# Kernel optimization log

Measured on AMD Instinct MI355X. Metric: run time of the kernel, lower is better.

## Reference

```python
import jax, jax.numpy as jnp
import numpy as np

B, N, D = 2, 2048, 1024
H, DH = 16, 64
INNER = H * DH  # 1024
EPS = 1e-5


def setup_inputs() -> dict:
    key = jax.random.key(0)
    ks = jax.random.split(key, 7)
    x = jax.random.normal(ks[0], (B, N, D), dtype=jnp.float32)
    mask = jax.random.uniform(ks[1], (B, N)) < 0.9
    mask = mask.at[:, 0].set(True)  # guarantee at least one valid key per row
    attn_bias = jax.random.normal(ks[2], (H, N, N), dtype=jnp.float32) * 0.02
    ln_w = jnp.ones((D,), dtype=jnp.float32)
    ln_b = jnp.zeros((D,), dtype=jnp.float32)
    wq = jax.random.normal(ks[3], (D, INNER), dtype=jnp.float32) * 0.02
    wkv = jax.random.normal(ks[4], (D, 2 * DH), dtype=jnp.float32) * 0.02
    wo = jax.random.normal(ks[5], (INNER, D), dtype=jnp.float32) * 0.02
    return {"x": x, "attn_bias": attn_bias, "ln_w": ln_w, "ln_b": ln_b,
            "wq": wq, "wkv": wkv, "wo": wo, "mask": mask}


def reference(x, attn_bias, ln_w, ln_b, wq, wkv, wo, mask):
    scale = DH ** -0.5
    # NOTE: in the torch module, kv_input = x BEFORE self.norm (context=None),
    # so K/V come from raw x while Q comes from LayerNorm(x).
    mu = jnp.mean(x, axis=-1, keepdims=True)
    var = jnp.var(x, axis=-1, keepdims=True)
    xn = (x - mu) / jnp.sqrt(var + EPS) * ln_w + ln_b
    q = (xn @ wq).reshape(B, N, H, DH).transpose(0, 2, 1, 3) * scale  # b h n d
    kv = x @ wkv                     # b n 2*dh (shared single KV head, MQA)
    k, v = kv[..., :DH], kv[..., DH:]
    sim = jnp.einsum('bhid,bjd->bhij', q, k) + attn_bias  # bias broadcasts over b
    mask_value = -jnp.finfo(sim.dtype).max
    sim = jnp.where(mask[:, None, None, :], sim, mask_value)
    attn = jax.nn.softmax(sim, axis=-1)
    out = jnp.einsum('bhij,bjd->bhid', attn, v)
    out = out.transpose(0, 2, 1, 3).reshape(B, N, INNER)
    return out @ wo
```

## Files before the change

### kernel.cpp

```cpp
#include <hip/hip_runtime.h>
#include <hip/hip_bf16.h>

typedef __bf16 bf16_t;
typedef __bf16 bf16x4 __attribute__((ext_vector_type(4)));
typedef __bf16 bf16x8 __attribute__((ext_vector_type(8)));
typedef float f32x4 __attribute__((ext_vector_type(4)));

static constexpr int BB    = 2;
static constexpr int SEQ   = 2048;
static constexpr int DM    = 1024;
static constexpr int NHEAD = 16;
static constexpr int HD    = 64;
static constexpr float L2E = 1.4426950408889634f;

__device__ __forceinline__ bf16x8 ld8(const bf16_t* p) {
  return *reinterpret_cast<const bf16x8*>(p);
}

__device__ __forceinline__ void gl_lds16(const bf16_t* g, bf16_t* l) {
  __builtin_amdgcn_global_load_lds(
      (const __attribute__((address_space(1))) void*)g,
      (__attribute__((address_space(3))) void*)l, 16, 0, 0);
}

__device__ __forceinline__ uint2 shfl2(uint2 v, int src) {
  uint2 r;
  r.x = (unsigned)__shfl((int)v.x, src, 64);
  r.y = (unsigned)__shfl((int)v.y, src, 64);
  return r;
}

template <typename T> __device__ __forceinline__ T cvt_out(float v);
template <> __device__ __forceinline__ float  cvt_out<float >(float v) { return v; }
template <> __device__ __forceinline__ bf16_t cvt_out<bf16_t>(float v) { return (bf16_t)v; }

__global__ __launch_bounds__(256) void transpose_cast(const float* __restrict__ in,
                                                      bf16_t* __restrict__ out,
                                                      int R, int C) {
  __shared__ float tile[32][33];
  const int c0 = blockIdx.x * 32, r0 = blockIdx.y * 32;
  const int tx = threadIdx.x & 31, ty = threadIdx.x >> 5;
#pragma unroll
  for (int y = ty; y < 32; y += 8)
    tile[y][tx] = in[(size_t)(r0 + y) * C + (c0 + tx)];
  __syncthreads();
#pragma unroll
  for (int y = ty; y < 32; y += 8)
    out[(size_t)(c0 + y) * R + (r0 + tx)] = (bf16_t)tile[tx][y];
}

__global__ __launch_bounds__(256) void row_prep(const float* __restrict__ x,
    const float* __restrict__ ln_w, const float* __restrict__ ln_b,
    const int* __restrict__ mask,
    bf16_t* __restrict__ xbf, bf16_t* __restrict__ xn, float* __restrict__ maskA) {
  const int row = blockIdx.x, t = threadIdx.x;
  __shared__ float red[8];
  const float4 xv = *reinterpret_cast<const float4*>(&x[(size_t)row * DM + t * 4]);
  float s  = xv.x + xv.y + xv.z + xv.w;
  float s2 = xv.x * xv.x + xv.y * xv.y + xv.z * xv.z + xv.w * xv.w;
#pragma unroll
  for (int off = 32; off >= 1; off >>= 1) {
    s  += __shfl_xor(s,  off, 64);
    s2 += __shfl_xor(s2, off, 64);
  }
  if ((t & 63) == 0) { red[t >> 6] = s; red[4 + (t >> 6)] = s2; }
  __syncthreads();
  s  = red[0] + red[1] + red[2] + red[3];
  s2 = red[4] + red[5] + red[6] + red[7];
  const float mu   = s * (1.0f / DM);
  const float var  = s2 * (1.0f / DM) - mu * mu;
  const float rstd = rsqrtf(var + 1e-5f);
  const float4 wv = *reinterpret_cast<const float4*>(&ln_w[t * 4]);
  const float4 bv = *reinterpret_cast<const float4*>(&ln_b[t * 4]);
  union { bf16_t h[4]; uint2 u; } p0, p1;
  p0.h[0] = (bf16_t)xv.x; p0.h[1] = (bf16_t)xv.y;
  p0.h[2] = (bf16_t)xv.z; p0.h[3] = (bf16_t)xv.w;
  p1.h[0] = (bf16_t)((xv.x - mu) * rstd * wv.x + bv.x);
  p1.h[1] = (bf16_t)((xv.y - mu) * rstd * wv.y + bv.y);
  p1.h[2] = (bf16_t)((xv.z - mu) * rstd * wv.z + bv.z);
  p1.h[3] = (bf16_t)((xv.w - mu) * rstd * wv.w + bv.w);
  *reinterpret_cast<uint2*>(&xbf[(size_t)row * DM + t * 4]) = p0.u;
  *reinterpret_cast<uint2*>(&xn [(size_t)row * DM + t * 4]) = p1.u;
  if (t == 0) maskA[row] = mask[row] ? 0.0f : -1e30f;
}

template <typename OutT>
__global__ __launch_bounds__(256) void gemm128(const bf16_t* __restrict__ A,
    const bf16_t* __restrict__ Bt, OutT* __restrict__ C,
    int M, int Nn, int K, float scale) {
  __shared__ alignas(16) bf16_t As[128 * 32];
  __shared__ alignas(16) bf16_t Bs[128 * 32];
  const int m0 = blockIdx.x * 128, n0 = blockIdx.y * 128;
  const int t = threadIdx.x, lane = t & 63, w = t >> 6;
  const int wm = (w & 1) * 64, wn = (w >> 1) * 64;
  const int l15 = lane & 15, q4 = lane >> 4;
  f32x4 acc[4][4] = {};
  const int sr = lane >> 2, sc = (lane & 3) * 8;
  const bf16_t* Ap0 = A  + (size_t)(m0 + w * 32 + sr) * K + sc;
  const bf16_t* Ap1 = Ap0 + (size_t)16 * K;
  const bf16_t* Bp0 = Bt + (size_t)(n0 + w * 32 + sr) * K + sc;
  const bf16_t* Bp1 = Bp0 + (size_t)16 * K;
  bf16_t* AsL0 = &As[(w * 32) * 32];
  bf16_t* AsL1 = &As[(w * 32 + 16) * 32];
  bf16_t* BsL0 = &Bs[(w * 32) * 32];
  bf16_t* BsL1 = &Bs[(w * 32 + 16) * 32];
  for (int k0 = 0; k0 < K; k0 += 32) {
    gl_lds16(Ap0 + k0, AsL0);
    gl_lds16(Ap1 + k0, AsL1);
    gl_lds16(Bp0 + k0, BsL0);
    gl_lds16(Bp1 + k0, BsL1);
    __syncthreads();
    bf16x8 af[4], bfr[4];
#pragma unroll
    for (int mt = 0; mt < 4; ++mt) af[mt]  = ld8(&As[(wm + mt * 16 + l15) * 32 + q4 * 8]);
#pragma unroll
    for (int nt = 0; nt < 4; ++nt) bfr[nt] = ld8(&Bs[(wn + nt * 16 + l15) * 32 + q4 * 8]);
#pragma unroll
    for (int mt = 0; mt < 4; ++mt)
#pragma unroll
      for (int nt = 0; nt < 4; ++nt)
        acc[mt][nt] = __builtin_amdgcn_mfma_f32_16x16x32_bf16(af[mt], bfr[nt], acc[mt][nt], 0, 0, 0);
    __syncthreads();
  }
#pragma unroll
  for (int mt = 0; mt < 4; ++mt)
#pragma unroll
    for (int nt = 0; nt < 4; ++nt)
#pragma unroll
      for (int r = 0; r < 4; ++r) {
        const int gm = m0 + wm + mt * 16 + q4 * 4 + r;
        const int gn = n0 + wn + nt * 16 + l15;
        C[(size_t)gm * Nn + gn] = cvt_out<OutT>(acc[mt][nt][r] * scale);
      }
}

__global__ __launch_bounds__(256) void gemm_kv(const bf16_t* __restrict__ A,
    const bf16_t* __restrict__ Bt, bf16_t* __restrict__ C, bf16_t* __restrict__ C2,
    int M, int Nn, int K) {
  __shared__ alignas(16) bf16_t As[128 * 32];
  __shared__ alignas(16) bf16_t Bs[64 * 32];
  const int m0 = blockIdx.x * 128, n0 = blockIdx.y * 64;
  const int t = threadIdx.x, lane = t & 63, w = t >> 6;
  const int wm = (w & 1) * 64, wn = (w >> 1) * 32;
  const int l15 = lane & 15, q4 = lane >> 4;
  f32x4 acc[4][2] = {};
  const int sr = lane >> 2, sc = (lane & 3) * 8;
  const bf16_t* Ap0 = A  + (size_t)(m0 + w * 32 + sr) * K + sc;
  const bf16_t* Ap1 = Ap0 + (size_t)16 * K;
  const bf16_t* Bp  = Bt + (size_t)(n0 + w * 16 + sr) * K + sc;
  bf16_t* AsL0 = &As[(w * 32) * 32];
  bf16_t* AsL1 = &As[(w * 32 + 16) * 32];
  bf16_t* BsL  = &Bs[(w * 16) * 32];
  for (int k0 = 0; k0 < K; k0 += 32) {
    gl_lds16(Ap0 + k0, AsL0);
    gl_lds16(Ap1 + k0, AsL1);
    gl_lds16(Bp  + k0, BsL);
    __syncthreads();
    bf16x8 af[4], bfr[2];
#pragma unroll
    for (int mt = 0; mt < 4; ++mt) af[mt]  = ld8(&As[(wm + mt * 16 + l15) * 32 + q4 * 8]);
#pragma unroll
    for (int nt = 0; nt < 2; ++nt) bfr[nt] = ld8(&Bs[(wn + nt * 16 + l15) * 32 + q4 * 8]);
#pragma unroll
    for (int mt = 0; mt < 4; ++mt)
#pragma unroll
      for (int nt = 0; nt < 2; ++nt)
        acc[mt][nt] = __builtin_amdgcn_mfma_f32_16x16x32_bf16(af[mt], bfr[nt], acc[mt][nt], 0, 0, 0);
    __syncthreads();
  }
#pragma unroll
  for (int mt = 0; mt < 4; ++mt)
#pragma unroll
    for (int nt = 0; nt < 2; ++nt)
#pragma unroll
      for (int r = 0; r < 4; ++r) {
        const int gm = m0 + wm + mt * 16 + q4 * 4 + r;
        const int gn = n0 + wn + nt * 16 + l15;
        const bf16_t ov = (bf16_t)acc[mt][nt][r];
        if (gn < HD) C[(size_t)gm * HD + gn] = ov;
        else C2[((size_t)(gm >> 11) * HD + (gn - HD)) * SEQ + (gm & 2047)] = ov;
      }
}

__global__ __launch_bounds__(256, 4) void flash_attn(
    const bf16_t* __restrict__ q,
    const bf16_t* __restrict__ kk,
    const bf16_t* __restrict__ vT,
    const float*  __restrict__ bias,
    const float*  __restrict__ maskA,
    bf16_t* __restrict__ aout)
{
  const int b = blockIdx.y & 1, h = blockIdx.y >> 1;
  const int i0 = blockIdx.x * 64;
  const int t = threadIdx.x, lane = t & 63, w = t >> 6;
  const int l15 = lane & 15, q4 = lane >> 4;

  __shared__ alignas(16) bf16_t Ks[2][64][72];
  __shared__ alignas(16) bf16_t Vs[2][64][72];

  const bf16_t* qrow = &q[((size_t)b * SEQ + i0 + w * 16 + l15) * DM + h * HD];
  const bf16x8 bq0 = ld8(qrow + q4 * 8);
  const bf16x8 bq1 = ld8(qrow + 32 + q4 * 8);

  f32x4 o[4] = {};
  float m_run = -1e30f, l_run = 0.0f;

  const float* bias_p = bias + (size_t)h * SEQ * SEQ
                      + (size_t)(i0 + w * 16 + l15) * SEQ + q4 * 4;
  const float* mask_p = maskA + b * SEQ + q4 * 4;

  const int sr = t >> 2, sc = (t & 3) * 16;
  const bf16_t* kp = &kk[((size_t)b * SEQ + sr) * HD + sc];
  const bf16_t* vp = &vT[((size_t)b * HD + sr) * SEQ + sc];

  uint4 kr0 = *reinterpret_cast<const uint4*>(kp);
  uint4 kr1 = *reinterpret_cast<const uint4*>(kp + 8);
  uint4 vr0 = *reinterpret_cast<const uint4*>(vp);
  uint4 vr1 = *reinterpret_cast<const uint4*>(vp + 8);
  f32x4 bv[4], mv[4];
#pragma unroll
  for (int mt = 0; mt < 4; ++mt) {
    bv[mt] = *reinterpret_cast<const f32x4*>(bias_p + mt * 16);
    mv[mt] = *reinterpret_cast<const f32x4*>(mask_p + mt * 16);
  }
  *reinterpret_cast<uint4*>(&Ks[0][sr][sc])     = kr0;
  *reinterpret_cast<uint4*>(&Ks[0][sr][sc + 8]) = kr1;
  *reinterpret_cast<uint4*>(&Vs[0][sr][sc])     = vr0;
  *reinterpret_cast<uint4*>(&Vs[0][sr][sc + 8]) = vr1;
  __syncthreads();

  for (int it = 0; it < SEQ / 64; ++it) {
    const int buf = it & 1;
    const int j1 = (it + 1) * 64;
    const bool more = (j1 < SEQ);
    if (more) {
      kr0 = *reinterpret_cast<const uint4*>(kp + (size_t)j1 * HD);
      kr1 = *reinterpret_cast<const uint4*>(kp + (size_t)j1 * HD + 8);
      vr0 = *reinterpret_cast<const uint4*>(vp + j1);
      vr1 = *reinterpret_cast<const uint4*>(vp + j1 + 8);
    }

    f32x4 s[4];
#pragma unroll
    for (int mt = 0; mt < 4; ++mt) {
      const bf16x8 a0 = ld8(&Ks[buf][mt * 16 + l15][q4 * 8]);
      const bf16x8 a1 = ld8(&Ks[buf][mt * 16 + l15][32 + q4 * 8]);
      f32x4 z = {0.f, 0.f, 0.f, 0.f};
      z = __builtin_amdgcn_mfma_f32_16x16x32_bf16(a0, bq0, z, 0, 0, 0);
      z = __builtin_amdgcn_mfma_f32_16x16x32_bf16(a1, bq1, z, 0, 0, 0);
      s[mt] = z;
    }

    float mx = -1e30f;
#pragma unroll
    for (int mt = 0; mt < 4; ++mt)
#pragma unroll
      for (int r = 0; r < 4; ++r) {
        s[mt][r] = s[mt][r] + bv[mt][r] + mv[mt][r];
        mx = fmaxf(mx, s[mt][r]);
      }
    if (more) {
#pragma unroll
      for (int mt = 0; mt < 4; ++mt) {
        bv[mt] = *reinterpret_cast<const f32x4*>(bias_p + j1 + mt * 16);
        mv[mt] = *reinterpret_cast<const f32x4*>(mask_p + j1 + mt * 16);
      }
    }
    mx = fmaxf(mx, __shfl_xor(mx, 16, 64));
    mx = fmaxf(mx, __shfl_xor(mx, 32, 64));
    const float mnew  = fmaxf(m_run, mx);
    const float alpha = __builtin_amdgcn_exp2f((m_run - mnew) * L2E);
    const float cc    = -mnew * L2E;
    m_run = mnew;

    float su = 0.0f;
#pragma unroll
    for (int mt = 0; mt < 4; ++mt)
#pragma unroll
      for (int r = 0; r < 4; ++r) {
        s[mt][r] = __builtin_amdgcn_exp2f(__builtin_fmaf(s[mt][r], L2E, cc));
        su += s[mt][r];
      }
    su += __shfl_xor(su, 16, 64);
    su += __shfl_xor(su, 32, 64);
    l_run = l_run * alpha + su;

#pragma unroll
    for (int r = 0; r < 4; ++r) {
      const float a_r = __shfl(alpha, q4 * 4 + r, 64);
      o[0][r] *= a_r; o[1][r] *= a_r; o[2][r] *= a_r; o[3][r] *= a_r;
    }

    uint2 pk[4];
#pragma unroll
    for (int mt = 0; mt < 4; ++mt) {
      union { bf16_t hh[4]; uint2 u; } pu;
      pu.hh[0] = (bf16_t)s[mt][0]; pu.hh[1] = (bf16_t)s[mt][1];
      pu.hh[2] = (bf16_t)s[mt][2]; pu.hh[3] = (bf16_t)s[mt][3];
      pk[mt] = pu.u;
    }
    const int src0 = ((q4 & 1) << 5) + l15;
    const int src1 = src0 + 16;
    const bool hiSel = (q4 >> 1) != 0;
#pragma unroll
    for (int ks = 0; ks < 2; ++ks) {
      const uint2 a0 = shfl2(pk[2 * ks],     src0);
      const uint2 a1 = shfl2(pk[2 * ks + 1], src0);
      const uint2 b0 = shfl2(pk[2 * ks],     src1);
      const uint2 b1 = shfl2(pk[2 * ks + 1], src1);
      union { unsigned u[4]; bf16x8 v; } pf;
      pf.u[0] = hiSel ? a1.x : a0.x; pf.u[1] = hiSel ? a1.y : a0.y;
      pf.u[2] = hiSel ? b1.x : b0.x; pf.u[3] = hiSel ? b1.y : b0.y;
#pragma unroll
      for (int nt = 0; nt < 4; ++nt) {
        const bf16x8 vv = ld8(&Vs[buf][nt * 16 + l15][ks * 32 + q4 * 8]);
        o[nt] = __builtin_amdgcn_mfma_f32_16x16x32_bf16(pf.v, vv, o[nt], 0, 0, 0);
      }
    }

    if (more) {
      *reinterpret_cast<uint4*>(&Ks[buf ^ 1][sr][sc])     = kr0;
      *reinterpret_cast<uint4*>(&Ks[buf ^ 1][sr][sc + 8]) = kr1;
      *reinterpret_cast<uint4*>(&Vs[buf ^ 1][sr][sc])     = vr0;
      *reinterpret_cast<uint4*>(&Vs[buf ^ 1][sr][sc + 8]) = vr1;
    }
    __syncthreads();
  }

#pragma unroll
  for (int r = 0; r < 4; ++r) {
    const float linv = 1.0f / __shfl(l_run, q4 * 4 + r, 64);
    const int gi = i0 + w * 16 + q4 * 4 + r;
    bf16_t* dst = &aout[((size_t)b * SEQ + gi) * DM + h * HD];
#pragma unroll
    for (int nt = 0; nt < 4; ++nt)
      dst[nt * 16 + l15] = (bf16_t)(o[nt][r] * linv);
  }
}

extern "C" void kernel_launch(void* const* d_in, const int* in_sizes, int n_in,
                              void* d_out, int out_size, void* d_ws, size_t ws_size,
                              hipStream_t stream) {
  const float* x         = (const float*)d_in[0];
  const float* attn_bias = (const float*)d_in[1];
  const float* ln_w      = (const float*)d_in[2];
  const float* ln_b      = (const float*)d_in[3];
  const float* wq        = (const float*)d_in[4];
  const float* wkv       = (const float*)d_in[5];
  const float* wo        = (const float*)d_in[6];
  const int*   mask      = (const int*)d_in[7];
  float* out = (float*)d_out;

  char* ws = (char*)d_ws;
  size_t off = 0;
  auto alloc = [&](size_t bytes) {
    char* p = ws + off;
    off += (bytes + 255) & ~(size_t)255;
    return p;
  };
  bf16_t* xbf   = (bf16_t*)alloc((size_t)BB * SEQ * DM * 2);
  bf16_t* xn    = (bf16_t*)alloc((size_t)BB * SEQ * DM * 2);
  bf16_t* wqT   = (bf16_t*)alloc((size_t)DM * DM * 2);
  bf16_t* wkvT  = (bf16_t*)alloc((size_t)2 * HD * DM * 2);
  bf16_t* woT   = (bf16_t*)alloc((size_t)DM * DM * 2);
  bf16_t* qb    = (bf16_t*)alloc((size_t)BB * SEQ * DM * 2);
  bf16_t* kkb   = (bf16_t*)alloc((size_t)BB * SEQ * HD * 2);
  bf16_t* vTb   = (bf16_t*)alloc((size_t)BB * HD * SEQ * 2);
  bf16_t* aoutb = (bf16_t*)alloc((size_t)BB * SEQ * DM * 2);
  float*  maskA = (float*)alloc((size_t)BB * SEQ * 4);

  transpose_cast<<<dim3(DM / 32, DM / 32), 256, 0, stream>>>(wq, wqT, DM, DM);
  transpose_cast<<<dim3(128 / 32, DM / 32), 256, 0, stream>>>(wkv, wkvT, DM, 128);
  transpose_cast<<<dim3(DM / 32, DM / 32), 256, 0, stream>>>(wo, woT, DM, DM);
  row_prep<<<BB * SEQ, 256, 0, stream>>>(x, ln_w, ln_b, mask, xbf, xn, maskA);
  gemm128<bf16_t><<<dim3(32, 8), 256, 0, stream>>>(xn, wqT, qb, BB * SEQ, DM, DM, 0.125f);
  gemm_kv<<<dim3(32, 2), 256, 0, stream>>>(xbf, wkvT, kkb, vTb, BB * SEQ, 128, DM);
  flash_attn<<<dim3(SEQ / 64, BB * NHEAD), 256, 0, stream>>>(qb, kkb, vTb, attn_bias,
                                                             maskA, aoutb);
  gemm128<float><<<dim3(32, 8), 256, 0, stream>>>(aoutb, woT, out, BB * SEQ, DM, DM, 1.0f);
}
```

Before: 512.2 us.

## Process both batches per attention block to share bias loads

Each flash-attention block now handles both batch elements for one head and query tile, so every attn_bias tile is loaded once and used twice. This halves the grid, doubles the per-block K/V staging and register state, and drops the K/V prefetch double buffering in favour of a single buffer per batch guarded by two barriers per iteration. The P-matrix relayout moves from cross-lane shuffles to a per-warp LDS scratch tile, and launch bounds fall from 4 to 3 blocks per SM to allow more registers. The gain on bias traffic comes at the cost of less latency hiding and lower occupancy.

```diff
diff --git a/kernel.cpp b/kernel.cpp
--- a/kernel.cpp
+++ b/kernel.cpp
@@ -21,13 +21,6 @@
   __builtin_amdgcn_global_load_lds(
       (const __attribute__((address_space(1))) void*)g,
       (__attribute__((address_space(3))) void*)l, 16, 0, 0);
-}
-
-__device__ __forceinline__ uint2 shfl2(uint2 v, int src) {
-  uint2 r;
-  r.x = (unsigned)__shfl((int)v.x, src, 64);
-  r.y = (unsigned)__shfl((int)v.y, src, 64);
-  return r;
 }
 
 template <typename T> __device__ __forceinline__ T cvt_out(float v);
@@ -182,7 +175,7 @@
       }
 }
 
-__global__ __launch_bounds__(256, 4) void flash_attn(
+__global__ __launch_bounds__(256, 3) void flash_attn(
     const bf16_t* __restrict__ q,
     const bf16_t* __restrict__ kk,
     const bf16_t* __restrict__ vT,
@@ -190,152 +183,171 @@
     const float*  __restrict__ maskA,
     bf16_t* __restrict__ aout)
 {
-  const int b = blockIdx.y & 1, h = blockIdx.y >> 1;
+  const int h  = blockIdx.y;
   const int i0 = blockIdx.x * 64;
   const int t = threadIdx.x, lane = t & 63, w = t >> 6;
   const int l15 = lane & 15, q4 = lane >> 4;
 
   __shared__ alignas(16) bf16_t Ks[2][64][72];
   __shared__ alignas(16) bf16_t Vs[2][64][72];
-
-  const bf16_t* qrow = &q[((size_t)b * SEQ + i0 + w * 16 + l15) * DM + h * HD];
-  const bf16x8 bq0 = ld8(qrow + q4 * 8);
-  const bf16x8 bq1 = ld8(qrow + 32 + q4 * 8);
-
-  f32x4 o[4] = {};
-  float m_run = -1e30f, l_run = 0.0f;
+  __shared__ alignas(16) bf16_t Pt[4][16][72];
+
+  bf16x8 bq[2][2];
+#pragma unroll
+  for (int b = 0; b < 2; ++b) {
+    const bf16_t* qrow = &q[((size_t)b * SEQ + i0 + w * 16 + l15) * DM + h * HD];
+    bq[b][0] = ld8(qrow + q4 * 8);
+    bq[b][1] = ld8(qrow + 32 + q4 * 8);
+  }
+
+  f32x4 o[2][4] = {};
+  float m_run[2] = {-1e30f, -1e30f};
+  float l_run[2] = {0.0f, 0.0f};
 
   const float* bias_p = bias + (size_t)h * SEQ * SEQ
                       + (size_t)(i0 + w * 16 + l15) * SEQ + q4 * 4;
-  const float* mask_p = maskA + b * SEQ + q4 * 4;
 
   const int sr = t >> 2, sc = (t & 3) * 16;
-  const bf16_t* kp = &kk[((size_t)b * SEQ + sr) * HD + sc];
-  const bf16_t* vp = &vT[((size_t)b * HD + sr) * SEQ + sc];
-
-  uint4 kr0 = *reinterpret_cast<const uint4*>(kp);
-  uint4 kr1 = *reinterpret_cast<const uint4*>(kp + 8);
-  uint4 vr0 = *reinterpret_cast<const uint4*>(vp);
-  uint4 vr1 = *reinterpret_cast<const uint4*>(vp + 8);
-  f32x4 bv[4], mv[4];
-#pragma unroll
-  for (int mt = 0; mt < 4; ++mt) {
-    bv[mt] = *reinterpret_cast<const f32x4*>(bias_p + mt * 16);
-    mv[mt] = *reinterpret_cast<const f32x4*>(mask_p + mt * 16);
-  }
-  *reinterpret_cast<uint4*>(&Ks[0][sr][sc])     = kr0;
-  *reinterpret_cast<uint4*>(&Ks[0][sr][sc + 8]) = kr1;
-  *reinterpret_cast<uint4*>(&Vs[0][sr][sc])     = vr0;
-  *reinterpret_cast<uint4*>(&Vs[0][sr][sc + 8]) = vr1;
+  const bf16_t* kp[2];
+  const bf16_t* vp[2];
+#pragma unroll
+  for (int b = 0; b < 2; ++b) {
+    kp[b] = &kk[((size_t)b * SEQ + sr) * HD + sc];
+    vp[b] = &vT[((size_t)b * HD + sr) * SEQ + sc];
+  }
+
+  uint4 kr[2][2], vr[2][2];
+#pragma unroll
+  for (int b = 0; b < 2; ++b) {
+    kr[b][0] = *reinterpret_cast<const uint4*>(kp[b]);
+    kr[b][1] = *reinterpret_cast<const uint4*>(kp[b] + 8);
+    vr[b][0] = *reinterpret_cast<const uint4*>(vp[b]);
+    vr[b][1] = *reinterpret_cast<const uint4*>(vp[b] + 8);
+  }
+#pragma unroll
+  for (int b = 0; b < 2; ++b) {
+    *reinterpret_cast<uint4*>(&Ks[b][sr][sc])     = kr[b][0];
+    *reinterpret_cast<uint4*>(&Ks[b][sr][sc + 8]) = kr[b][1];
+    *reinterpret_cast<uint4*>(&Vs[b][sr][sc])     = vr[b][0];
+    *reinterpret_cast<uint4*>(&Vs[b][sr][sc + 8]) = vr[b][1];
+  }
   __syncthreads();
 
   for (int it = 0; it < SEQ / 64; ++it) {
-    const int buf = it & 1;
-    const int j1 = (it + 1) * 64;
+    const int j0 = it * 64;
+    const int j1 = j0 + 64;
     const bool more = (j1 < SEQ);
     if (more) {
-      kr0 = *reinterpret_cast<const uint4*>(kp + (size_t)j1 * HD);
-      kr1 = *reinterpret_cast<const uint4*>(kp + (size_t)j1 * HD + 8);
-      vr0 = *reinterpret_cast<const uint4*>(vp + j1);
-      vr1 = *reinterpret_cast<const uint4*>(vp + j1 + 8);
+#pragma unroll
+      for (int b = 0; b < 2; ++b) {
+        kr[b][0] = *reinterpret_cast<const uint4*>(kp[b] + (size_t)j1 * HD);
+        kr[b][1] = *reinterpret_cast<const uint4*>(kp[b] + (size_t)j1 * HD + 8);
+        vr[b][0] = *reinterpret_cast<const uint4*>(vp[b] + j1);
+        vr[b][1] = *reinterpret_cast<const uint4*>(vp[b] + j1 + 8);
+      }
     }
 
-    f32x4 s[4];
-#pragma unroll
-    for (int mt = 0; mt < 4; ++mt) {
-      const bf16x8 a0 = ld8(&Ks[buf][mt * 16 + l15][q4 * 8]);
-      const bf16x8 a1 = ld8(&Ks[buf][mt * 16 + l15][32 + q4 * 8]);
-      f32x4 z = {0.f, 0.f, 0.f, 0.f};
-      z = __builtin_amdgcn_mfma_f32_16x16x32_bf16(a0, bq0, z, 0, 0, 0);
-      z = __builtin_amdgcn_mfma_f32_16x16x32_bf16(a1, bq1, z, 0, 0, 0);
-      s[mt] = z;
+    f32x4 bv[4];
+#pragma unroll
+    for (int mt = 0; mt < 4; ++mt)
+      bv[mt] = *reinterpret_cast<const f32x4*>(bias_p + j0 + mt * 16);
+
+    f32x4 s[2][4];
+#pragma unroll
+    for (int b = 0; b < 2; ++b)
+#pragma unroll
+      for (int mt = 0; mt < 4; ++mt) {
+        const bf16x8 a0 = ld8(&Ks[b][mt * 16 + l15][q4 * 8]);
+        const bf16x8 a1 = ld8(&Ks[b][mt * 16 + l15][32 + q4 * 8]);
+        f32x4 z = {0.f, 0.f, 0.f, 0.f};
+        z = __builtin_amdgcn_mfma_f32_16x16x32_bf16(a0, bq[b][0], z, 0, 0, 0);
+        z = __builtin_amdgcn_mfma_f32_16x16x32_bf16(a1, bq[b][1], z, 0, 0, 0);
+        s[b][mt] = z;
+      }
+
+#pragma unroll
+    for (int b = 0; b < 2; ++b) {
+      f32x4 mv[4];
+#pragma unroll
+      for (int mt = 0; mt < 4; ++mt)
+        mv[mt] = *reinterpret_cast<const f32x4*>(maskA + b * SEQ + j0 + mt * 16 + q4 * 4);
+
+      float mx = -1e30f;
+#pragma unroll
+      for (int mt = 0; mt < 4; ++mt)
+#pragma unroll
+        for (int r = 0; r < 4; ++r) {
+          s[b][mt][r] = s[b][mt][r] + bv[mt][r] + mv[mt][r];
+          mx = fmaxf(mx, s[b][mt][r]);
+        }
+      mx = fmaxf(mx, __shfl_xor(mx, 16, 64));
+      mx = fmaxf(mx, __shfl_xor(mx, 32, 64));
+      const float mnew  = fmaxf(m_run[b], mx);
+      const float alpha = __builtin_amdgcn_exp2f((m_run[b] - mnew) * L2E);
+      const float cc    = -mnew * L2E;
+      m_run[b] = mnew;
+
+      float su = 0.0f;
+#pragma unroll
+      for (int mt = 0; mt < 4; ++mt)
+#pragma unroll
+        for (int r = 0; r < 4; ++r) {
+          s[b][mt][r] = __builtin_amdgcn_exp2f(__builtin_fmaf(s[b][mt][r], L2E, cc));
+          su += s[b][mt][r];
+        }
+      su += __shfl_xor(su, 16, 64);
+      su += __shfl_xor(su, 32, 64);
+      l_run[b] = l_run[b] * alpha + su;
+
+#pragma unroll
+      for (int mt = 0; mt < 4; ++mt) {
+        union { bf16_t hh[4]; uint2 u; } pu;
+        pu.hh[0] = (bf16_t)s[b][mt][0]; pu.hh[1] = (bf16_t)s[b][mt][1];
+        pu.hh[2] = (bf16_t)s[b][mt][2]; pu.hh[3] = (bf16_t)s[b][mt][3];
+        *reinterpret_cast<uint2*>(&Pt[w][l15][mt * 16 + q4 * 4]) = pu.u;
+      }
+
+#pragma unroll
+      for (int r = 0; r < 4; ++r) {
+        const float a_r = __shfl(alpha, q4 * 4 + r, 64);
+        o[b][0][r] *= a_r; o[b][1][r] *= a_r; o[b][2][r] *= a_r; o[b][3][r] *= a_r;
+      }
+
+#pragma unroll
+      for (int ks = 0; ks < 2; ++ks) {
+        const bf16x8 pf = ld8(&Pt[w][l15][ks * 32 + q4 * 8]);
+#pragma unroll
+        for (int nt = 0; nt < 4; ++nt) {
+          const bf16x8 vv = ld8(&Vs[b][nt * 16 + l15][ks * 32 + q4 * 8]);
+          o[b][nt] = __builtin_amdgcn_mfma_f32_16x16x32_bf16(pf, vv, o[b][nt], 0, 0, 0);
+        }
+      }
     }
 
-    float mx = -1e30f;
-#pragma unroll
-    for (int mt = 0; mt < 4; ++mt)
-#pragma unroll
-      for (int r = 0; r < 4; ++r) {
-        s[mt][r] = s[mt][r] + bv[mt][r] + mv[mt][r];
-        mx = fmaxf(mx, s[mt][r]);
-      }
+    __syncthreads();
     if (more) {
 #pragma unroll
-      for (int mt = 0; mt < 4; ++mt) {
-        bv[mt] = *reinterpret_cast<const f32x4*>(bias_p + j1 + mt * 16);
-        mv[mt] = *reinterpret_cast<const f32x4*>(mask_p + j1 + mt * 16);
+      for (int b = 0; b < 2; ++b) {
+        *reinterpret_cast<uint4*>(&Ks[b][sr][sc])     = kr[b][0];
+        *reinterpret_cast<uint4*>(&Ks[b][sr][sc + 8]) = kr[b][1];
+        *reinterpret_cast<uint4*>(&Vs[b][sr][sc])     = vr[b][0];
+        *reinterpret_cast<uint4*>(&Vs[b][sr][sc + 8]) = vr[b][1];
       }
     }
-    mx = fmaxf(mx, __shfl_xor(mx, 16, 64));
-    mx = fmaxf(mx, __shfl_xor(mx, 32, 64));
-    const float mnew  = fmaxf(m_run, mx);
-    const float alpha = __builtin_amdgcn_exp2f((m_run - mnew) * L2E);
-    const float cc    = -mnew * L2E;
-    m_run = mnew;
-
-    float su = 0.0f;
-#pragma unroll
-    for (int mt = 0; mt < 4; ++mt)
-#pragma unroll
-      for (int r = 0; r < 4; ++r) {
-        s[mt][r] = __builtin_amdgcn_exp2f(__builtin_fmaf(s[mt][r], L2E, cc));
-        su += s[mt][r];
-      }
-    su += __shfl_xor(su, 16, 64);
-    su += __shfl_xor(su, 32, 64);
-    l_run = l_run * alpha + su;
-
+    __syncthreads();
+  }
+
+#pragma unroll
+  for (int b = 0; b < 2; ++b)
 #pragma unroll
     for (int r = 0; r < 4; ++r) {
-      const float a_r = __shfl(alpha, q4 * 4 + r, 64);
-      o[0][r] *= a_r; o[1][r] *= a_r; o[2][r] *= a_r; o[3][r] *= a_r;
+      const float linv = 1.0f / __shfl(l_run[b], q4 * 4 + r, 64);
+      const int gi = i0 + w * 16 + q4 * 4 + r;
+      bf16_t* dst = &aout[((size_t)b * SEQ + gi) * DM + h * HD];
+#pragma unroll
+      for (int nt = 0; nt < 4; ++nt)
+        dst[nt * 16 + l15] = (bf16_t)(o[b][nt][r] * linv);
     }
-
-    uint2 pk[4];
-#pragma unroll
-    for (int mt = 0; mt < 4; ++mt) {
-      union { bf16_t hh[4]; uint2 u; } pu;
-      pu.hh[0] = (bf16_t)s[mt][0]; pu.hh[1] = (bf16_t)s[mt][1];
-      pu.hh[2] = (bf16_t)s[mt][2]; pu.hh[3] = (bf16_t)s[mt][3];
-      pk[mt] = pu.u;
-    }
-    const int src0 = ((q4 & 1) << 5) + l15;
-    const int src1 = src0 + 16;
-    const bool hiSel = (q4 >> 1) != 0;
-#pragma unroll
-    for (int ks = 0; ks < 2; ++ks) {
-      const uint2 a0 = shfl2(pk[2 * ks],     src0);
-      const uint2 a1 = shfl2(pk[2 * ks + 1], src0);
-      const uint2 b0 = shfl2(pk[2 * ks],     src1);
-      const uint2 b1 = shfl2(pk[2 * ks + 1], src1);
-      union { unsigned u[4]; bf16x8 v; } pf;
-      pf.u[0] = hiSel ? a1.x : a0.x; pf.u[1] = hiSel ? a1.y : a0.y;
-      pf.u[2] = hiSel ? b1.x : b0.x; pf.u[3] = hiSel ? b1.y : b0.y;
-#pragma unroll
-      for (int nt = 0; nt < 4; ++nt) {
-        const bf16x8 vv = ld8(&Vs[buf][nt * 16 + l15][ks * 32 + q4 * 8]);
-        o[nt] = __builtin_amdgcn_mfma_f32_16x16x32_bf16(pf.v, vv, o[nt], 0, 0, 0);
-      }
-    }
-
-    if (more) {
-      *reinterpret_cast<uint4*>(&Ks[buf ^ 1][sr][sc])     = kr0;
-      *reinterpret_cast<uint4*>(&Ks[buf ^ 1][sr][sc + 8]) = kr1;
-      *reinterpret_cast<uint4*>(&Vs[buf ^ 1][sr][sc])     = vr0;
-      *reinterpret_cast<uint4*>(&Vs[buf ^ 1][sr][sc + 8]) = vr1;
-    }
-    __syncthreads();
-  }
-
-#pragma unroll
-  for (int r = 0; r < 4; ++r) {
-    const float linv = 1.0f / __shfl(l_run, q4 * 4 + r, 64);
-    const int gi = i0 + w * 16 + q4 * 4 + r;
-    bf16_t* dst = &aout[((size_t)b * SEQ + gi) * DM + h * HD];
-#pragma unroll
-    for (int nt = 0; nt < 4; ++nt)
-      dst[nt * 16 + l15] = (bf16_t)(o[nt][r] * linv);
-  }
 }
 
 extern "C" void kernel_launch(void* const* d_in, const int* in_sizes, int n_in,
@@ -375,7 +387,7 @@
   row_prep<<<BB * SEQ, 256, 0, stream>>>(x, ln_w, ln_b, mask, xbf, xn, maskA);
   gemm128<bf16_t><<<dim3(32, 8), 256, 0, stream>>>(xn, wqT, qb, BB * SEQ, DM, DM, 0.125f);
   gemm_kv<<<dim3(32, 2), 256, 0, stream>>>(xbf, wkvT, kkb, vTb, BB * SEQ, 128, DM);
-  flash_attn<<<dim3(SEQ / 64, BB * NHEAD), 256, 0, stream>>>(qb, kkb, vTb, attn_bias,
-                                                             maskA, aoutb);
+  flash_attn<<<dim3(SEQ / 64, NHEAD), 256, 0, stream>>>(qb, kkb, vTb, attn_bias,
+                                                        maskA, aoutb);
   gemm128<float><<<dim3(32, 8), 256, 0, stream>>>(aoutb, woT, out, BB * SEQ, DM, DM, 1.0f);
 }
```

After: 671.8 us. 1.31x slower.

## Merge both batches into one 512-thread attention block sharing bias tiles

Applied to the files above, without the earlier changes.

The flash attention kernel now launches one 512-thread block per (query tile, head) that covers both batches. Each group of four waves handles one batch and owns one K/V LDS buffer, so the two batches' loads of the same attn_bias rows can hit in cache together. This targets the fp32 bias stream, which dominates traffic because it is read once per batch. In exchange the K/V double buffering and bias/mask register prefetch are dropped, an extra barrier is added per iteration, and the grid has half as many blocks.

```diff
diff --git a/kernel.cpp b/kernel.cpp
--- a/kernel.cpp
+++ b/kernel.cpp
@@ -182,7 +182,7 @@
       }
 }
 
-__global__ __launch_bounds__(256, 4) void flash_attn(
+__global__ __launch_bounds__(512, 4) void flash_attn(
     const bf16_t* __restrict__ q,
     const bf16_t* __restrict__ kk,
     const bf16_t* __restrict__ vT,
@@ -190,15 +190,17 @@
     const float*  __restrict__ maskA,
     bf16_t* __restrict__ aout)
 {
-  const int b = blockIdx.y & 1, h = blockIdx.y >> 1;
+  const int h  = blockIdx.y;
   const int i0 = blockIdx.x * 64;
   const int t = threadIdx.x, lane = t & 63, w = t >> 6;
+  const int bg = w >> 2;
+  const int wl = w & 3;
   const int l15 = lane & 15, q4 = lane >> 4;
 
   __shared__ alignas(16) bf16_t Ks[2][64][72];
   __shared__ alignas(16) bf16_t Vs[2][64][72];
 
-  const bf16_t* qrow = &q[((size_t)b * SEQ + i0 + w * 16 + l15) * DM + h * HD];
+  const bf16_t* qrow = &q[((size_t)bg * SEQ + i0 + wl * 16 + l15) * DM + h * HD];
   const bf16x8 bq0 = ld8(qrow + q4 * 8);
   const bf16x8 bq1 = ld8(qrow + 32 + q4 * 8);
 
@@ -206,32 +208,27 @@
   float m_run = -1e30f, l_run = 0.0f;
 
   const float* bias_p = bias + (size_t)h * SEQ * SEQ
-                      + (size_t)(i0 + w * 16 + l15) * SEQ + q4 * 4;
-  const float* mask_p = maskA + b * SEQ + q4 * 4;
-
-  const int sr = t >> 2, sc = (t & 3) * 16;
-  const bf16_t* kp = &kk[((size_t)b * SEQ + sr) * HD + sc];
-  const bf16_t* vp = &vT[((size_t)b * HD + sr) * SEQ + sc];
+                      + (size_t)(i0 + wl * 16 + l15) * SEQ + q4 * 4;
+  const float* mask_p = maskA + bg * SEQ + q4 * 4;
+
+  const int tl = t & 255;
+  const int sr = tl >> 2, sc = (tl & 3) * 16;
+  const bf16_t* kp = &kk[((size_t)bg * SEQ + sr) * HD + sc];
+  const bf16_t* vp = &vT[((size_t)bg * HD + sr) * SEQ + sc];
 
   uint4 kr0 = *reinterpret_cast<const uint4*>(kp);
   uint4 kr1 = *reinterpret_cast<const uint4*>(kp + 8);
   uint4 vr0 = *reinterpret_cast<const uint4*>(vp);
   uint4 vr1 = *reinterpret_cast<const uint4*>(vp + 8);
-  f32x4 bv[4], mv[4];
-#pragma unroll
-  for (int mt = 0; mt < 4; ++mt) {
-    bv[mt] = *reinterpret_cast<const f32x4*>(bias_p + mt * 16);
-    mv[mt] = *reinterpret_cast<const f32x4*>(mask_p + mt * 16);
-  }
-  *reinterpret_cast<uint4*>(&Ks[0][sr][sc])     = kr0;
-  *reinterpret_cast<uint4*>(&Ks[0][sr][sc + 8]) = kr1;
-  *reinterpret_cast<uint4*>(&Vs[0][sr][sc])     = vr0;
-  *reinterpret_cast<uint4*>(&Vs[0][sr][sc + 8]) = vr1;
+  *reinterpret_cast<uint4*>(&Ks[bg][sr][sc])     = kr0;
+  *reinterpret_cast<uint4*>(&Ks[bg][sr][sc + 8]) = kr1;
+  *reinterpret_cast<uint4*>(&Vs[bg][sr][sc])     = vr0;
+  *reinterpret_cast<uint4*>(&Vs[bg][sr][sc + 8]) = vr1;
   __syncthreads();
 
   for (int it = 0; it < SEQ / 64; ++it) {
-    const int buf = it & 1;
-    const int j1 = (it + 1) * 64;
+    const int j0 = it * 64;
+    const int j1 = j0 + 64;
     const bool more = (j1 < SEQ);
     if (more) {
       kr0 = *reinterpret_cast<const uint4*>(kp + (size_t)j1 * HD);
@@ -240,11 +237,16 @@
       vr1 = *reinterpret_cast<const uint4*>(vp + j1 + 8);
     }
 
+    f32x4 bv[4];
+#pragma unroll
+    for (int mt = 0; mt < 4; ++mt)
+      bv[mt] = *reinterpret_cast<const f32x4*>(bias_p + j0 + mt * 16);
+
     f32x4 s[4];
 #pragma unroll
     for (int mt = 0; mt < 4; ++mt) {
-      const bf16x8 a0 = ld8(&Ks[buf][mt * 16 + l15][q4 * 8]);
-      const bf16x8 a1 = ld8(&Ks[buf][mt * 16 + l15][32 + q4 * 8]);
+      const bf16x8 a0 = ld8(&Ks[bg][mt * 16 + l15][q4 * 8]);
+      const bf16x8 a1 = ld8(&Ks[bg][mt * 16 + l15][32 + q4 * 8]);
       f32x4 z = {0.f, 0.f, 0.f, 0.f};
       z = __builtin_amdgcn_mfma_f32_16x16x32_bf16(a0, bq0, z, 0, 0, 0);
       z = __builtin_amdgcn_mfma_f32_16x16x32_bf16(a1, bq1, z, 0, 0, 0);
@@ -253,17 +255,12 @@
 
     float mx = -1e30f;
 #pragma unroll
-    for (int mt = 0; mt < 4; ++mt)
+    for (int mt = 0; mt < 4; ++mt) {
+      const f32x4 mv = *reinterpret_cast<const f32x4*>(mask_p + j0 + mt * 16);
 #pragma unroll
       for (int r = 0; r < 4; ++r) {
-        s[mt][r] = s[mt][r] + bv[mt][r] + mv[mt][r];
+        s[mt][r] = s[mt][r] + bv[mt][r] + mv[r];
         mx = fmaxf(mx, s[mt][r]);
-      }
-    if (more) {
-#pragma unroll
-      for (int mt = 0; mt < 4; ++mt) {
-        bv[mt] = *reinterpret_cast<const f32x4*>(bias_p + j1 + mt * 16);
-        mv[mt] = *reinterpret_cast<const f32x4*>(mask_p + j1 + mt * 16);
       }
     }
     mx = fmaxf(mx, __shfl_xor(mx, 16, 64));
@@ -313,16 +310,17 @@
       pf.u[2] = hiSel ? b1.x : b0.x; pf.u[3] = hiSel ? b1.y : b0.y;
 #pragma unroll
       for (int nt = 0; nt < 4; ++nt) {
-        const bf16x8 vv = ld8(&Vs[buf][nt * 16 + l15][ks * 32 + q4 * 8]);
+        const bf16x8 vv = ld8(&Vs[bg][nt * 16 + l15][ks * 32 + q4 * 8]);
         o[nt] = __builtin_amdgcn_mfma_f32_16x16x32_bf16(pf.v, vv, o[nt], 0, 0, 0);
       }
     }
 
+    __syncthreads();
     if (more) {
-      *reinterpret_cast<uint4*>(&Ks[buf ^ 1][sr][sc])     = kr0;
-      *reinterpret_cast<uint4*>(&Ks[buf ^ 1][sr][sc + 8]) = kr1;
-      *reinterpret_cast<uint4*>(&Vs[buf ^ 1][sr][sc])     = vr0;
-      *reinterpret_cast<uint4*>(&Vs[buf ^ 1][sr][sc + 8]) = vr1;
+      *reinterpret_cast<uint4*>(&Ks[bg][sr][sc])     = kr0;
+      *reinterpret_cast<uint4*>(&Ks[bg][sr][sc + 8]) = kr1;
+      *reinterpret_cast<uint4*>(&Vs[bg][sr][sc])     = vr0;
+      *reinterpret_cast<uint4*>(&Vs[bg][sr][sc + 8]) = vr1;
     }
     __syncthreads();
   }
@@ -330,8 +328,8 @@
 #pragma unroll
   for (int r = 0; r < 4; ++r) {
     const float linv = 1.0f / __shfl(l_run, q4 * 4 + r, 64);
-    const int gi = i0 + w * 16 + q4 * 4 + r;
-    bf16_t* dst = &aout[((size_t)b * SEQ + gi) * DM + h * HD];
+    const int gi = i0 + wl * 16 + q4 * 4 + r;
+    bf16_t* dst = &aout[((size_t)bg * SEQ + gi) * DM + h * HD];
 #pragma unroll
     for (int nt = 0; nt < 4; ++nt)
       dst[nt * 16 + l15] = (bf16_t)(o[nt][r] * linv);
@@ -375,7 +373,7 @@
   row_prep<<<BB * SEQ, 256, 0, stream>>>(x, ln_w, ln_b, mask, xbf, xn, maskA);
   gemm128<bf16_t><<<dim3(32, 8), 256, 0, stream>>>(xn, wqT, qb, BB * SEQ, DM, DM, 0.125f);
   gemm_kv<<<dim3(32, 2), 256, 0, stream>>>(xbf, wkvT, kkb, vTb, BB * SEQ, 128, DM);
-  flash_attn<<<dim3(SEQ / 64, BB * NHEAD), 256, 0, stream>>>(qb, kkb, vTb, attn_bias,
-                                                             maskA, aoutb);
+  flash_attn<<<dim3(SEQ / 64, NHEAD), 512, 0, stream>>>(qb, kkb, vTb, attn_bias,
+                                                        maskA, aoutb);
   gemm128<float><<<dim3(32, 8), 256, 0, stream>>>(aoutb, woT, out, BB * SEQ, DM, DM, 1.0f);
 }
```

Result: slower. 537.8 us (+5.0%).
